# Optimization experiments

Hardware: AMD Instinct MI355X
Metric: run time of the kernel (lower is better)

The kernel has to match this reference:

```python
import jax, jax.numpy as jnp
import numpy as np

NPOINT, RADIUS, NSAMPLE = 2048, 0.2, 32
BN_EPS = 1e-5


def _fps(xyz, npoint):
    # Farthest point sampling. xyz: [B,N,3] -> idx [B,npoint] (int32).
    B, N, _ = xyz.shape
    def step(carry, _):
        dist, farthest = carry  # dist [B,N], farthest [B]
        centroid = xyz[jnp.arange(B), farthest]            # [B,3]
        d = jnp.sum((xyz - centroid[:, None, :]) ** 2, -1)  # [B,N]
        dist = jnp.minimum(dist, d)
        nxt = jnp.argmax(dist, axis=-1).astype(jnp.int32)
        return (dist, nxt), farthest
    init = (jnp.full((B, N), 1e10, xyz.dtype), jnp.zeros((B,), jnp.int32))
    _, idxs = jax.lax.scan(step, init, None, length=npoint)
    return jnp.transpose(idxs)  # [B, npoint]


def _ball_query(radius, nsample, xyz, new_xyz):
    # xyz [B,N,3], new_xyz [B,S,3] -> idx [B,S,nsample]
    B, N, _ = xyz.shape
    sqr = jnp.sum((new_xyz[:, :, None, :] - xyz[:, None, :, :]) ** 2, -1)  # [B,S,N]
    ar = jnp.arange(N, dtype=jnp.int32)[None, None, :]
    idx = jnp.where(sqr > radius * radius, N, ar)
    idx = jnp.sort(idx, axis=-1)[..., :nsample]
    first = idx[..., :1]
    return jnp.where(idx == N, first, idx)


def _index_points(points, idx):
    # points [B,N,C], idx [B,...] -> [B,...,C]
    B = points.shape[0]
    bidx = jnp.arange(B).reshape((B,) + (1,) * (idx.ndim - 1))
    return points[bidx, idx]


def _mlp_layer(x, w, b, g, bt):
    # 1x1 Conv2d over [B,S,K,Cin] + inference BatchNorm (mean=0, var=1) + ReLU
    z = jnp.einsum('bskc,oc->bsko', x, w) + b
    z = g * (z / jnp.sqrt(1.0 + BN_EPS)) + bt
    return jax.nn.relu(z)


def setup_inputs():
    key = jax.random.key(0)
    ks = jax.random.split(key, 8)
    B, N, C = 8, 8192, 64
    inp = {
        'xyz': jax.random.uniform(ks[0], (B, N, 3), jnp.float32),
        'feats': jax.random.normal(ks[1], (B, N, C), jnp.float32),
    }
    dims = [C + 3, 64, 64, 128]
    for i in range(3):
        cin, cout = dims[i], dims[i + 1]
        inp[f'w{i+1}'] = jax.random.normal(ks[2 + i], (cout, cin), jnp.float32) / np.float32(np.sqrt(cin))
        inp[f'b{i+1}'] = jnp.zeros((cout,), jnp.float32)
        inp[f'g{i+1}'] = jnp.ones((cout,), jnp.float32)
        inp[f'bt{i+1}'] = jnp.zeros((cout,), jnp.float32)
    return inp


def reference(xyz, feats, w1, b1, g1, bt1, w2, b2, g2, bt2, w3, b3, g3, bt3):
    center_idx = _fps(xyz, NPOINT)                 # [B,S]
    new_xyz = _index_points(xyz, center_idx)       # [B,S,3]
    idx = _ball_query(RADIUS, NSAMPLE, xyz, new_xyz)  # [B,S,K]
    grouped_xyz = _index_points(xyz, idx)          # [B,S,K,3]
    grouped_dp = (grouped_xyz - new_xyz[:, :, None, :]) / RADIUS  # normalize_dp
    grouped_feats = _index_points(feats, idx)      # [B,S,K,C]
    grouped = jnp.concatenate([grouped_dp, grouped_feats], axis=-1)  # [B,S,K,C+3]
    x = _mlp_layer(grouped, w1, b1, g1, bt1)
    x = _mlp_layer(x, w2, b2, g2, bt2)
    x = _mlp_layer(x, w3, b3, g3, bt3)
    new_feats = jnp.max(x, axis=2)                 # max over neighbors -> [B,S,Cout]
    return new_xyz, new_feats
```

## Files before the change

kernel.cpp:

```cpp
#include <hip/hip_runtime.h>
#include <cstdint>

typedef unsigned short u16;
typedef _Float16 f16x8  __attribute__((ext_vector_type(8)));
typedef float    f32x4  __attribute__((ext_vector_type(4)));
typedef float    v2f    __attribute__((ext_vector_type(2)));

#define DEV static __device__ __forceinline__

constexpr int kB = 8;
constexpr int kN = 8192;
constexpr int kS = 2048;
constexpr int kK = 32;
constexpr int kC = 64;

DEV v2f vmin2(v2f a, v2f b){ v2f r; r.x = fminf(a.x,b.x); r.y = fminf(a.y,b.y); return r; }

template<int CTRL>
DEV float dppmax(float v){
  int x = __builtin_amdgcn_mov_dpp(__builtin_bit_cast(int, v), CTRL, 0xF, 0xF, true);
  float o = __builtin_bit_cast(float, x);
  return fmaxf(v, o);
}
DEV float readlanef(float v, int l){
  return __builtin_bit_cast(float, __builtin_amdgcn_readlane(__builtin_bit_cast(int, v), l));
}

__global__ __launch_bounds__(256) void prep_kernel(const float* __restrict__ xyz,
                                                   float* __restrict__ X,
                                                   float* __restrict__ Y,
                                                   float* __restrict__ Z){
  int i = blockIdx.x * 256 + threadIdx.x;
  if (i < kB * kN){
    X[i] = xyz[i*3+0];
    Y[i] = xyz[i*3+1];
    Z[i] = xyz[i*3+2];
  }
}

__global__ __launch_bounds__(512) __attribute__((amdgpu_waves_per_eu(2, 2)))
void fps_kernel(const float* __restrict__ X,
                const float* __restrict__ Y,
                const float* __restrict__ Z,
                int* __restrict__ cidx,
                float* __restrict__ oxyz){
  __shared__ __align__(16) float lx[kN];
  __shared__ __align__(16) float ly[kN];
  __shared__ __align__(16) float lz[kN];
  __shared__ uint64_t sk[2][8];
  const int b    = blockIdx.x;
  const int tid  = threadIdx.x;
  const int lane = tid & 63;
  const int wid  = tid >> 6;
  const float* xb = X + b*kN;
  const float* yb = Y + b*kN;
  const float* zb = Z + b*kN;

  v2f px[8], py[8], pz[8], dd[8];
  const int p0 = tid*16;
  {
    f32x4 t0 = *(const f32x4*)(xb+p0);   f32x4 t1 = *(const f32x4*)(xb+p0+4);
    f32x4 t2 = *(const f32x4*)(xb+p0+8); f32x4 t3 = *(const f32x4*)(xb+p0+12);
    *(f32x4*)(lx+p0)=t0; *(f32x4*)(lx+p0+4)=t1; *(f32x4*)(lx+p0+8)=t2; *(f32x4*)(lx+p0+12)=t3;
    px[0]=(v2f){t0.x,t0.y}; px[1]=(v2f){t0.z,t0.w}; px[2]=(v2f){t1.x,t1.y}; px[3]=(v2f){t1.z,t1.w};
    px[4]=(v2f){t2.x,t2.y}; px[5]=(v2f){t2.z,t2.w}; px[6]=(v2f){t3.x,t3.y}; px[7]=(v2f){t3.z,t3.w};
  }
  {
    f32x4 t0 = *(const f32x4*)(yb+p0);   f32x4 t1 = *(const f32x4*)(yb+p0+4);
    f32x4 t2 = *(const f32x4*)(yb+p0+8); f32x4 t3 = *(const f32x4*)(yb+p0+12);
    *(f32x4*)(ly+p0)=t0; *(f32x4*)(ly+p0+4)=t1; *(f32x4*)(ly+p0+8)=t2; *(f32x4*)(ly+p0+12)=t3;
    py[0]=(v2f){t0.x,t0.y}; py[1]=(v2f){t0.z,t0.w}; py[2]=(v2f){t1.x,t1.y}; py[3]=(v2f){t1.z,t1.w};
    py[4]=(v2f){t2.x,t2.y}; py[5]=(v2f){t2.z,t2.w}; py[6]=(v2f){t3.x,t3.y}; py[7]=(v2f){t3.z,t3.w};
  }
  {
    f32x4 t0 = *(const f32x4*)(zb+p0);   f32x4 t1 = *(const f32x4*)(zb+p0+4);
    f32x4 t2 = *(const f32x4*)(zb+p0+8); f32x4 t3 = *(const f32x4*)(zb+p0+12);
    *(f32x4*)(lz+p0)=t0; *(f32x4*)(lz+p0+4)=t1; *(f32x4*)(lz+p0+8)=t2; *(f32x4*)(lz+p0+12)=t3;
    pz[0]=(v2f){t0.x,t0.y}; pz[1]=(v2f){t0.z,t0.w}; pz[2]=(v2f){t1.x,t1.y}; pz[3]=(v2f){t1.z,t1.w};
    pz[4]=(v2f){t2.x,t2.y}; pz[5]=(v2f){t2.z,t2.w}; pz[6]=(v2f){t3.x,t3.y}; pz[7]=(v2f){t3.z,t3.w};
  }
  #pragma unroll
  for (int j = 0; j < 8; j++){ dd[j].x = 1e10f; dd[j].y = 1e10f; }

  __syncthreads();
  float cx = lx[0], cy = ly[0], cz = lz[0];
  if (tid == 0){
    cidx[b*kS] = 0;
    size_t o = (size_t)b*kS*3;
    oxyz[o+0] = cx; oxyz[o+1] = cy; oxyz[o+2] = cz;
  }

  #pragma unroll 1
  for (int t = 1; t < kS; t++){
    float q[8];
    {
      #pragma clang fp contract(off)
      v2f c2x; c2x.x = cx; c2x.y = cx;
      v2f c2y; c2y.x = cy; c2y.y = cy;
      v2f c2z; c2z.x = cz; c2z.y = cz;
      #pragma unroll
      for (int j = 0; j < 8; j++){
        v2f dx = px[j] - c2x;
        v2f dy = py[j] - c2y;
        v2f dz = pz[j] - c2z;
        v2f d  = dx*dx + dy*dy;
        d = d + dz*dz;
        dd[j] = vmin2(dd[j], d);
        q[j]  = fmaxf(dd[j].x, dd[j].y);
      }
    }
    float m0 = fmaxf(q[0], q[1]);
    float m1 = fmaxf(q[2], q[3]);
    float m2 = fmaxf(q[4], q[5]);
    float m3 = fmaxf(q[6], q[7]);
    float lmax = fmaxf(fmaxf(m0, m1), fmaxf(m2, m3));
    int sl = 0;
    #pragma unroll
    for (int j = 7; j >= 0; j--){
      if (dd[j].y == lmax) sl = 2*j + 1;
      if (dd[j].x == lmax) sl = 2*j;
    }
    float r = lmax;
    r = dppmax<0xB1>(r);
    r = dppmax<0x4E>(r);
    r = dppmax<0x114>(r);
    r = dppmax<0x118>(r);
    r = dppmax<0x142>(r);
    r = dppmax<0x143>(r);
    float wmax = readlanef(r, 63);
    unsigned long long mk = __ballot(lmax == wmax);
    int wl   = (int)__builtin_ctzll(mk);
    int widx = __builtin_amdgcn_readlane(tid*16 + sl, wl);
    if (lane == 0)
      sk[t & 1][wid] = ((uint64_t)__builtin_bit_cast(uint32_t, wmax) << 32)
                     | (uint32_t)widx;
    __syncthreads();
    uint64_t kk = sk[t & 1][lane & 7];
    float m8 = __builtin_bit_cast(float, (uint32_t)(kk >> 32));
    int   i8 = (int)(uint32_t)kk;
    float r2 = m8;
    r2 = dppmax<0xB1>(r2);
    r2 = dppmax<0x4E>(r2);
    r2 = dppmax<0x114>(r2);
    float bmax = readlanef(r2, 7);
    unsigned long long mk2 = __ballot(m8 == bmax);
    int ww = (int)__builtin_ctzll(mk2);
    int w  = __builtin_amdgcn_readlane(i8, ww);
    cx = lx[w]; cy = ly[w]; cz = lz[w];
    if (tid == 0){
      cidx[b*kS + t] = w;
      size_t o = ((size_t)b*kS + t) * 3;
      oxyz[o+0] = cx; oxyz[o+1] = cy; oxyz[o+2] = cz;
    }
  }
}

__global__ __launch_bounds__(256) void ballq_kernel(const float* __restrict__ X,
                                                    const float* __restrict__ Y,
                                                    const float* __restrict__ Z,
                                                    const int* __restrict__ cidx,
                                                    u16* __restrict__ bidx){
  const int lw   = threadIdx.x >> 6;
  const int lane = threadIdx.x & 63;
  const int wv   = blockIdx.x * 4 + lw;
  __shared__ u16 buf[4][kK];
  const int b = wv >> 11;
  const float* xb = X + b*kN;
  const float* yb = Y + b*kN;
  const float* zb = Z + b*kN;
  const int ci = cidx[wv];
  const float ccx = xb[ci], ccy = yb[ci], ccz = zb[ci];
  const float R2 = (float)(0.2*0.2);

  int cnt = 0;
  for (int base = 0; base < kN; base += 64){
    float sq;
    {
      #pragma clang fp contract(off)
      int p = base + lane;
      float dx = xb[p] - ccx;
      float dy = yb[p] - ccy;
      float dz = zb[p] - ccz;
      sq = dx*dx + dy*dy;
      sq = sq + dz*dz;
    }
    bool in = !(sq > R2);
    unsigned long long mk = __ballot(in);
    int pos = cnt + __popcll(mk & ((1ull << lane) - 1ull));
    if (in && pos < kK) buf[lw][pos] = (u16)(base + lane);
    cnt += (int)__popcll(mk);
    if (cnt >= kK) break;
  }
  u16 first = buf[lw][0];
  if (lane < kK){
    int c = cnt < kK ? cnt : kK;
    bidx[(size_t)wv*kK + lane] = (lane < c) ? buf[lw][lane] : first;
  }
}

DEV f16x8 ld8cvt(const float* p){
  f32x4 a = *(const f32x4*)p;
  f32x4 b = *(const f32x4*)(p + 4);
  f16x8 h;
  #pragma unroll
  for (int j = 0; j < 4; j++){ h[j] = (_Float16)a[j]; h[4+j] = (_Float16)b[j]; }
  return h;
}

__global__ __launch_bounds__(256) void mlp_kernel(
    const float* __restrict__ feats,
    const float* __restrict__ w1, const float* __restrict__ b1, const float* __restrict__ g1, const float* __restrict__ bt1,
    const float* __restrict__ w2, const float* __restrict__ b2, const float* __restrict__ g2, const float* __restrict__ bt2,
    const float* __restrict__ w3, const float* __restrict__ b3, const float* __restrict__ g3, const float* __restrict__ bt3,
    const float* __restrict__ X, const float* __restrict__ Y, const float* __restrict__ Z,
    const int* __restrict__ cidx, const u16* __restrict__ bidx,
    float* __restrict__ ofeat)
{
  constexpr int HP = 72;
  __shared__ _Float16 H[4][32*HP];
  const int lw   = threadIdx.x >> 6;
  const int lane = threadIdx.x & 63;
  const int nl   = lane & 15;
  const int kg   = lane >> 4;
  const int gw   = blockIdx.x * 4 + lw;
  const float INVS = 0.99999500003749968f;

  f16x8 wf1[4][3];
  #pragma unroll
  for (int nt = 0; nt < 4; nt++){
    #pragma unroll
    for (int kt = 0; kt < 3; kt++){
      f16x8 h;
      #pragma unroll
      for (int j = 0; j < 8; j++){
        int k = kt*32 + kg*8 + j;
        int c = (k < 64) ? (k + 3) : ((k < 67) ? (k - 64) : -1);
        h[j] = (c >= 0) ? (_Float16)w1[(nt*16 + nl)*67 + c] : (_Float16)0.0f;
      }
      wf1[nt][kt] = h;
    }
  }
  f16x8 wf2[4][2];
  #pragma unroll
  for (int nt = 0; nt < 4; nt++)
    #pragma unroll
    for (int kt = 0; kt < 2; kt++)
      wf2[nt][kt] = ld8cvt(w2 + (nt*16 + nl)*64 + kt*32 + kg*8);
  f16x8 wf3[8][2];
  #pragma unroll
  for (int nt = 0; nt < 8; nt++)
    #pragma unroll
    for (int kt = 0; kt < 2; kt++)
      wf3[nt][kt] = ld8cvt(w3 + (nt*16 + nl)*64 + kt*32 + kg*8);

  float a1c[4], e1c[4], a2c[4], e2c[4], a3c[8], e3c[8];
  #pragma unroll
  for (int nt = 0; nt < 4; nt++){
    int c = nt*16 + nl;
    a1c[nt] = g1[c] * INVS; e1c[nt] = fmaf(a1c[nt], b1[c], bt1[c]);
    a2c[nt] = g2[c] * INVS; e2c[nt] = fmaf(a2c[nt], b2[c], bt2[c]);
  }
  #pragma unroll
  for (int nt = 0; nt < 8; nt++){
    int c = nt*16 + nl;
    a3c[nt] = g3[c] * INVS; e3c[nt] = fmaf(a3c[nt], b3[c], bt3[c]);
  }

  _Float16* Hw = &H[lw][0];
  const f32x4 z4 = {0.f, 0.f, 0.f, 0.f};

  #pragma unroll 1
  for (int i = 0; i < 8; i++){
    const int cid = gw*8 + i;
    const int b   = cid >> 11;
    const float* fb = feats + (size_t)b * kN * kC;

    int my = (int)bidx[(size_t)cid*kK + (lane & 31)];
    int n0 = __shfl(my, nl);
    int n1 = __shfl(my, 16 + nl);
    f16x8 a00 = ld8cvt(fb + (size_t)n0*kC +      kg*8);
    f16x8 a01 = ld8cvt(fb + (size_t)n0*kC + 32 + kg*8);
    f16x8 a10 = ld8cvt(fb + (size_t)n1*kC +      kg*8);
    f16x8 a11 = ld8cvt(fb + (size_t)n1*kC + 32 + kg*8);
    const float* xb = X + b*kN; const float* yb = Y + b*kN; const float* zb = Z + b*kN;
    int ci = cidx[cid];
    float ccx = xb[ci], ccy = yb[ci], ccz = zb[ci];
    float dpx = (xb[my] - ccx) / 0.2f;
    float dpy = (yb[my] - ccy) / 0.2f;
    float dpz = (zb[my] - ccz) / 0.2f;
    float x0 = __shfl(dpx, nl),      y0 = __shfl(dpy, nl),      zz0 = __shfl(dpz, nl);
    float x1 = __shfl(dpx, 16 + nl), y1 = __shfl(dpy, 16 + nl), zz1 = __shfl(dpz, 16 + nl);
    f16x8 ad0 = {0,0,0,0,0,0,0,0}, ad1 = {0,0,0,0,0,0,0,0};
    if (kg == 0){
      ad0[0] = (_Float16)x0; ad0[1] = (_Float16)y0; ad0[2] = (_Float16)zz0;
      ad1[0] = (_Float16)x1; ad1[1] = (_Float16)y1; ad1[2] = (_Float16)zz1;
    }

    f32x4 c1[2][4];
    #pragma unroll
    for (int nt = 0; nt < 4; nt++){
      f32x4 acc = z4;
      acc = __builtin_amdgcn_mfma_f32_16x16x32_f16(ad0, wf1[nt][2], acc, 0, 0, 0);
      acc = __builtin_amdgcn_mfma_f32_16x16x32_f16(a00, wf1[nt][0], acc, 0, 0, 0);
      acc = __builtin_amdgcn_mfma_f32_16x16x32_f16(a01, wf1[nt][1], acc, 0, 0, 0);
      c1[0][nt] = acc;
      acc = z4;
      acc = __builtin_amdgcn_mfma_f32_16x16x32_f16(ad1, wf1[nt][2], acc, 0, 0, 0);
      acc = __builtin_amdgcn_mfma_f32_16x16x32_f16(a10, wf1[nt][0], acc, 0, 0, 0);
      acc = __builtin_amdgcn_mfma_f32_16x16x32_f16(a11, wf1[nt][1], acc, 0, 0, 0);
      c1[1][nt] = acc;
    }
    #pragma unroll
    for (int mt = 0; mt < 2; mt++)
      #pragma unroll
      for (int nt = 0; nt < 4; nt++)
        #pragma unroll
        for (int r = 0; r < 4; r++){
          float h = fmaxf(fmaf(a1c[nt], c1[mt][nt][r], e1c[nt]), 0.f);
          Hw[(mt*16 + kg*4 + r)*HP + nt*16 + nl] = (_Float16)h;
        }
    f16x8 h1[2][2];
    #pragma unroll
    for (int mt = 0; mt < 2; mt++)
      #pragma unroll
      for (int kt = 0; kt < 2; kt++)
        h1[mt][kt] = *(const f16x8*)(Hw + (mt*16 + nl)*HP + kt*32 + kg*8);
    f32x4 c2[2][4];
    #pragma unroll
    for (int mt = 0; mt < 2; mt++)
      #pragma unroll
      for (int nt = 0; nt < 4; nt++){
        f32x4 acc = z4;
        acc = __builtin_amdgcn_mfma_f32_16x16x32_f16(h1[mt][0], wf2[nt][0], acc, 0, 0, 0);
        acc = __builtin_amdgcn_mfma_f32_16x16x32_f16(h1[mt][1], wf2[nt][1], acc, 0, 0, 0);
        c2[mt][nt] = acc;
      }
    #pragma unroll
    for (int mt = 0; mt < 2; mt++)
      #pragma unroll
      for (int nt = 0; nt < 4; nt++)
        #pragma unroll
        for (int r = 0; r < 4; r++){
          float h = fmaxf(fmaf(a2c[nt], c2[mt][nt][r], e2c[nt]), 0.f);
          Hw[(mt*16 + kg*4 + r)*HP + nt*16 + nl] = (_Float16)h;
        }
    f16x8 h2[2][2];
    #pragma unroll
    for (int mt = 0; mt < 2; mt++)
      #pragma unroll
      for (int kt = 0; kt < 2; kt++)
        h2[mt][kt] = *(const f16x8*)(Hw + (mt*16 + nl)*HP + kt*32 + kg*8);
    #pragma unroll
    for (int nt = 0; nt < 8; nt++){
      f32x4 d0 = z4, d1 = z4;
      d0 = __builtin_amdgcn_mfma_f32_16x16x32_f16(h2[0][0], wf3[nt][0], d0, 0, 0, 0);
      d0 = __builtin_amdgcn_mfma_f32_16x16x32_f16(h2[0][1], wf3[nt][1], d0, 0, 0, 0);
      d1 = __builtin_amdgcn_mfma_f32_16x16x32_f16(h2[1][0], wf3[nt][0], d1, 0, 0, 0);
      d1 = __builtin_amdgcn_mfma_f32_16x16x32_f16(h2[1][1], wf3[nt][1], d1, 0, 0, 0);
      float m = -1e30f;
      #pragma unroll
      for (int r = 0; r < 4; r++){
        m = fmaxf(m, fmaf(a3c[nt], d0[r], e3c[nt]));
        m = fmaxf(m, fmaf(a3c[nt], d1[r], e3c[nt]));
      }
      m = fmaxf(m, 0.f);
      m = fmaxf(m, __shfl_xor(m, 16));
      m = fmaxf(m, __shfl_xor(m, 32));
      if (lane < 16) ofeat[(size_t)cid*128 + nt*16 + nl] = m;
    }
  }
}

extern "C" void kernel_launch(void* const* d_in, const int* in_sizes, int n_in,
                              void* d_out, int out_size, void* d_ws, size_t ws_size,
                              hipStream_t stream){
  (void)in_sizes; (void)n_in; (void)out_size; (void)ws_size;
  const float* xyz   = (const float*)d_in[0];
  const float* feats = (const float*)d_in[1];
  const float* w1  = (const float*)d_in[2];
  const float* b1  = (const float*)d_in[3];
  const float* g1  = (const float*)d_in[4];
  const float* bt1 = (const float*)d_in[5];
  const float* w2  = (const float*)d_in[6];
  const float* b2  = (const float*)d_in[7];
  const float* g2  = (const float*)d_in[8];
  const float* bt2 = (const float*)d_in[9];
  const float* w3  = (const float*)d_in[10];
  const float* b3  = (const float*)d_in[11];
  const float* g3  = (const float*)d_in[12];
  const float* bt3 = (const float*)d_in[13];
  float* out = (float*)d_out;

  float* X  = (float*)d_ws;
  float* Y  = X + kB*kN;
  float* Z  = Y + kB*kN;
  int*   ci = (int*)(Z + kB*kN);
  u16*   bi = (u16*)(ci + kB*kS);

  hipLaunchKernelGGL(prep_kernel,  dim3(256),  dim3(256), 0, stream, xyz, X, Y, Z);
  hipLaunchKernelGGL(fps_kernel,   dim3(kB),   dim3(512), 0, stream, X, Y, Z, ci, out);
  hipLaunchKernelGGL(ballq_kernel, dim3(4096), dim3(256), 0, stream, X, Y, Z, ci, bi);
  hipLaunchKernelGGL(mlp_kernel,   dim3(512),  dim3(256), 0, stream,
                     feats, w1, b1, g1, bt1, w2, b2, g2, bt2, w3, b3, g3, bt3,
                     X, Y, Z, ci, bi, out + (size_t)kB*kS*3);
}
```

Before: 1.879 ms.

## Buffer FPS outputs in LDS and speculate centroid loads before reduction

```diff
diff --git a/kernel.cpp b/kernel.cpp
--- a/kernel.cpp
+++ b/kernel.cpp
@@ -47,6 +47,8 @@
   __shared__ __align__(16) float lx[kN];
   __shared__ __align__(16) float ly[kN];
   __shared__ __align__(16) float lz[kN];
+  __shared__ __align__(16) int   cl_i[kS];
+  __shared__ __align__(16) float cl_c[kS*3];
   __shared__ uint64_t sk[2][8];
   const int b    = blockIdx.x;
   const int tid  = threadIdx.x;
@@ -85,9 +87,8 @@
   __syncthreads();
   float cx = lx[0], cy = ly[0], cz = lz[0];
   if (tid == 0){
-    cidx[b*kS] = 0;
-    size_t o = (size_t)b*kS*3;
-    oxyz[o+0] = cx; oxyz[o+1] = cy; oxyz[o+2] = cz;
+    cl_i[0] = 0;
+    cl_c[0] = cx; cl_c[1] = cy; cl_c[2] = cz;
   }
 
   #pragma unroll 1
@@ -109,11 +110,10 @@
         q[j]  = fmaxf(dd[j].x, dd[j].y);
       }
     }
-    float m0 = fmaxf(q[0], q[1]);
-    float m1 = fmaxf(q[2], q[3]);
-    float m2 = fmaxf(q[4], q[5]);
-    float m3 = fmaxf(q[6], q[7]);
-    float lmax = fmaxf(fmaxf(m0, m1), fmaxf(m2, m3));
+    float lmax = fmaxf(fmaxf(q[0], q[1]), q[2]);
+    lmax = fmaxf(fmaxf(lmax, q[3]), q[4]);
+    lmax = fmaxf(fmaxf(lmax, q[5]), q[6]);
+    lmax = fmaxf(lmax, q[7]);
     int sl = 0;
     #pragma unroll
     for (int j = 7; j >= 0; j--){
@@ -138,6 +138,7 @@
     uint64_t kk = sk[t & 1][lane & 7];
     float m8 = __builtin_bit_cast(float, (uint32_t)(kk >> 32));
     int   i8 = (int)(uint32_t)kk;
+    float sx = lx[i8], sy = ly[i8], sz = lz[i8];
     float r2 = m8;
     r2 = dppmax<0xB1>(r2);
     r2 = dppmax<0x4E>(r2);
@@ -146,12 +147,23 @@
     unsigned long long mk2 = __ballot(m8 == bmax);
     int ww = (int)__builtin_ctzll(mk2);
     int w  = __builtin_amdgcn_readlane(i8, ww);
-    cx = lx[w]; cy = ly[w]; cz = lz[w];
+    cx = readlanef(sx, ww); cy = readlanef(sy, ww); cz = readlanef(sz, ww);
     if (tid == 0){
-      cidx[b*kS + t] = w;
-      size_t o = ((size_t)b*kS + t) * 3;
-      oxyz[o+0] = cx; oxyz[o+1] = cy; oxyz[o+2] = cz;
-    }
+      cl_i[t] = w;
+      cl_c[3*t+0] = cx; cl_c[3*t+1] = cy; cl_c[3*t+2] = cz;
+    }
+  }
+
+  __syncthreads();
+  #pragma unroll
+  for (int i = 0; i < kS/512; i++){
+    int s = i*512 + tid;
+    cidx[b*kS + s] = cl_i[s];
+  }
+  #pragma unroll
+  for (int i = 0; i < (kS*3)/512; i++){
+    int s = i*512 + tid;
+    oxyz[(size_t)b*kS*3 + s] = cl_c[s];
   }
 }
 
```

Result: no change. 1.889 ms (+0.5%).
